# Performance work log

Hardware: AMD Instinct MI355X
Metric: run time of the kernel (lower is better)

## Reference

```python
import jax, jax.numpy as jnp
import numpy as np

EPS = 1e-05
MOMENTUM = 0.1


def inv_sqrtm(A, eps=1e-09):
    # torch.svd: A = U diag(S) V^T ; jnp.linalg.svd: A = U diag(S) Vh, so Vh == V^T
    U, S, Vh = jnp.linalg.svd(A)
    S = jnp.maximum(S, eps)
    return (U * (S ** -0.5)[None, :]) @ Vh


def setup_inputs() -> dict:
    key = jax.random.key(0)
    N, d = 262144, 512
    x = jax.random.normal(key, (N, d), dtype=jnp.float32)
    running_covar = jnp.eye(d, dtype=jnp.float32)
    return {"x": x, "running_covar": running_covar}


def reference(x, running_covar):
    # training-mode BatchWhiten with track_running_stats=True, momentum=0.1
    N = x.shape[0]
    covar = (x.T @ x) / N                       # [d, d]
    eaf = MOMENTUM
    running = running_covar * eaf + covar * (1.0 - eaf)
    covar = jnp.maximum(running, EPS)           # elementwise max, as in torch.max(covar, eps)
    B = inv_sqrtm(covar, EPS)                   # [d, d] inverse sqrt via SVD
    return x @ B                                # whitened input [N, d]
```

## Files before the change

### kernel.cpp

```cpp
#include <hip/hip_runtime.h>
#include <stdint.h>


#define N_ROWS 262144
#define D 512
#define NS_ITERS 3
#define CK_CHUNKS 128
#define CK_ROWS (N_ROWS / CK_CHUNKS)
#define BKC 32
#define CK_STEPS (CK_ROWS / BKC)

typedef float f32x4 __attribute__((ext_vector_type(4)));
typedef short s16x8 __attribute__((ext_vector_type(8)));
typedef short s16x4 __attribute__((ext_vector_type(4)));
typedef __bf16 bf16x8 __attribute__((ext_vector_type(8)));

static __device__ __forceinline__ unsigned short f2bf(float f) {
  unsigned u = __float_as_uint(f);
  u += 0x7FFFu + ((u >> 16) & 1u);
  return (unsigned short)(u >> 16);
}

static __device__ __forceinline__ f32x4 mfma16(s16x8 a, s16x8 b, f32x4 c) {
  return __builtin_amdgcn_mfma_f32_16x16x32_bf16(
      __builtin_bit_cast(bf16x8, a), __builtin_bit_cast(bf16x8, b), c, 0, 0, 0);
}

static __device__ __forceinline__ void gld_lds16(const void* g, void* l) {
  __builtin_amdgcn_global_load_lds(
      (const __attribute__((address_space(1))) void*)g,
      (__attribute__((address_space(3))) void*)l, 16, 0, 0);
}

#define SWZ8(c) (((c) ^ ((c) >> 3)) & 7)

#define CVOFF(c, kc) \
  ((((c) >> 1) << 6) + ((((((kc) << 1) | ((c) & 1))) ^ SWZ8((c) >> 1)) << 3))

#define GSW(row, g) (((g) ^ (((row) >> 1) & 3)) << 3)

static __device__ __forceinline__ void bar_lgkm() {
  asm volatile("s_waitcnt lgkmcnt(0)" ::: "memory");
  __builtin_amdgcn_s_barrier();
  __builtin_amdgcn_sched_barrier(0);
}

__global__ __launch_bounds__(512) void covar_k(const float* __restrict__ x,
                                               float* __restrict__ Cpart,
                                               short* __restrict__ xb16) {
  __shared__ short ldsT[2][2][128 * 32];

  const int hw = blockIdx.x;
  const int work = (hw & 7) * 160 + (hw >> 3);
  int t = work % 10, mb = 0, rl = 4;
  while (t >= rl) { t -= rl; ++mb; --rl; }
  const int nb = mb + t;
  const int chunk = work / 10;
  float* C = Cpart + (size_t)(hw & 7) * (D * D);

  const int tid = threadIdx.x;
  const int lane = tid & 63;
  const int wave = tid >> 6;
  const int isB = wave >> 2;
  const int kh = wave & 3;
  const int c2 = lane * 2;

  const int wr = wave >> 2, wc = wave & 3;
  const int l15 = lane & 15, g = lane >> 4;

  const bool offd = (nb != mb);
  const bool doStage = (!isB) || offd;
  const int tileCol = (isB ? nb : mb) * 128;

  const bool haveDump = (xb16 != nullptr);
  const int rank = isB ? (4 - (nb - mb)) : (nb - mb);
  const bool dump = haveDump && doStage && (kh == rank);
  uint32_t* xw = (uint32_t*)xb16;

  f32x4 acc[4][2];
#pragma unroll
  for (int i = 0; i < 4; ++i)
#pragma unroll
    for (int j = 0; j < 2; ++j) acc[i][j] = f32x4{0.f, 0.f, 0.f, 0.f};

  const size_t kbase0 = (size_t)chunk * CK_ROWS;
  const float* srcBase = x + (kbase0 + kh * 8) * D + tileCol + c2;

  float2 buf[8];
  if (doStage) {
#pragma unroll
    for (int q = 0; q < 8; ++q) buf[q] = *(const float2*)(srcBase + (size_t)q * D);
  }

  for (int st = 0; st < CK_STEPS; ++st) {
    if (doStage) {
      s16x8 p0, p1;
#pragma unroll
      for (int q = 0; q < 8; ++q) {
        p0[q] = (short)f2bf(buf[q].x);
        p1[q] = (short)f2bf(buf[q].y);
      }
      if (st + 1 < CK_STEPS) {
        const float* src = srcBase + (size_t)(st + 1) * BKC * D;
#pragma unroll
        for (int q = 0; q < 8; ++q) buf[q] = *(const float2*)(src + (size_t)q * D);
      }
      short* wp = ldsT[st & 1][isB];
      *(s16x8*)(wp + CVOFF(c2, kh)) = p0;
      *(s16x8*)(wp + CVOFF(c2 + 1, kh)) = p1;
      if (dump) {
        const size_t k0 = kbase0 + (size_t)st * BKC;
#pragma unroll
        for (int q = 0; q < 8; ++q) {
          const uint32_t u =
              (uint32_t)(uint16_t)p0[q] | ((uint32_t)(uint16_t)p1[q] << 16);
          __builtin_nontemporal_store(
              u, &xw[(k0 + kh * 8 + q) * 256 + (tileCol >> 1) + lane]);
        }
      }
    }

    bar_lgkm();

    const short* rA = ldsT[st & 1][0];
    const short* rB = ldsT[st & 1][offd ? 1 : 0];
    s16x8 af[4], bfv[2];
#pragma unroll
    for (int mi = 0; mi < 4; ++mi) {
      const int m = 64 * wr + 16 * mi + l15;
      af[mi] = *(const s16x8*)(rA + CVOFF(m, g));
    }
#pragma unroll
    for (int nj = 0; nj < 2; ++nj) {
      const int n = 32 * wc + 16 * nj + l15;
      bfv[nj] = *(const s16x8*)(rB + CVOFF(n, g));
    }
#pragma unroll
    for (int mi = 0; mi < 4; ++mi)
#pragma unroll
      for (int nj = 0; nj < 2; ++nj)
        acc[mi][nj] = mfma16(af[mi], bfv[nj], acc[mi][nj]);
  }

#pragma unroll
  for (int mi = 0; mi < 4; ++mi)
#pragma unroll
    for (int nj = 0; nj < 2; ++nj) {
      const int n = nb * 128 + 32 * wc + 16 * nj + l15;
#pragma unroll
      for (int r = 0; r < 4; ++r) {
        const int m = mb * 128 + 64 * wr + 16 * mi + 4 * g + r;
        atomicAdd(&C[(size_t)m * D + n], acc[mi][nj][r]);
      }
    }
}

__global__ __launch_bounds__(256) void prep_k(const float* __restrict__ Cpart,
                                              const float* __restrict__ run,
                                              float* __restrict__ M,
                                              unsigned* __restrict__ sMax) {
  const int r = blockIdx.x;
  const int t = threadIdx.x;
  const float cs = 0.9f / (float)N_ROWS;
  float sum = 0.f;
  for (int c = t; c < D; c += 256) {
    const int rr = r < c ? r : c;
    const int cc = r < c ? c : r;
    float cv = 0.f;
#pragma unroll
    for (int p = 0; p < 8; ++p)
      cv += Cpart[(size_t)p * D * D + (size_t)rr * D + cc];
    float v = 0.1f * run[(size_t)r * D + c] + cs * cv;
    v = fmaxf(v, 1e-5f);
    M[(size_t)r * D + c] = v;
    sum += v;
  }
  __shared__ float red[256];
  red[t] = sum;
  __syncthreads();
  for (int off = 128; off > 0; off >>= 1) {
    if (t < off) red[t] += red[t + off];
    __syncthreads();
  }
  if (t == 0) atomicMax(sMax, __float_as_uint(red[0]));
}

__global__ __launch_bounds__(256) void init2_k(const float* __restrict__ M,
                                               const unsigned* __restrict__ sMax,
                                               float* __restrict__ Y0,
                                               float* __restrict__ T,
                                               float* __restrict__ Z1) {
  const float inv = 1.0f / __uint_as_float(*sMax);
  const int i0 = (blockIdx.x * 256 + threadIdx.x) * 4;
  const float4 m4 = *(const float4*)&M[i0];
  const int row = i0 >> 9, col0 = i0 & 511;
  float y[4], tv[4];
#pragma unroll
  for (int e = 0; e < 4; ++e) {
    y[e] = (&m4.x)[e] * inv;
    tv[e] = (row == col0 + e ? 1.5f : 0.f) - 0.5f * y[e];
  }
  *(float4*)&Y0[i0] = make_float4(y[0], y[1], y[2], y[3]);
  const float4 t4 = make_float4(tv[0], tv[1], tv[2], tv[3]);
  *(float4*)&T[i0] = t4;
  *(float4*)&Z1[i0] = t4;
}

__device__ __forceinline__ void mm512_body(const float* __restrict__ A,
                                           const float* __restrict__ B,
                                           float* a00, float* a01, float* a10,
                                           float* a11, int rbase, int cbase) {
  __shared__ float As[32][36];
  __shared__ float Bs[32][36];
  const int t = threadIdx.x;
  const int tx = t & 15, ty = t >> 4;
  const int sr = t >> 3, sc = (t & 7) * 4;
  float c00 = 0.f, c01 = 0.f, c10 = 0.f, c11 = 0.f;
  for (int k0 = 0; k0 < D; k0 += 32) {
    __syncthreads();
    *(float4*)&As[sr][sc] = *(const float4*)(A + (size_t)(rbase + sr) * D + k0 + sc);
    *(float4*)&Bs[sr][sc] = *(const float4*)(B + (size_t)(k0 + sr) * D + cbase + sc);
    __syncthreads();
#pragma unroll
    for (int kk = 0; kk < 32; ++kk) {
      const float av0 = As[2 * ty][kk], av1 = As[2 * ty + 1][kk];
      const float2 bv = *(const float2*)&Bs[kk][2 * tx];
      c00 = fmaf(av0, bv.x, c00);
      c01 = fmaf(av0, bv.y, c01);
      c10 = fmaf(av1, bv.x, c10);
      c11 = fmaf(av1, bv.y, c11);
    }
  }
  *a00 = c00; *a01 = c01; *a10 = c10; *a11 = c11;
}

__global__ __launch_bounds__(256) void mmY_k(const float* __restrict__ A,
                                             const float* __restrict__ B,
                                             float* __restrict__ O) {
  const int rbase = blockIdx.y * 32, cbase = blockIdx.x * 32;
  float a00, a01, a10, a11;
  mm512_body(A, B, &a00, &a01, &a10, &a11, rbase, cbase);
  const int tx = threadIdx.x & 15, ty = threadIdx.x >> 4;
  const int r0 = rbase + 2 * ty, c0 = cbase + 2 * tx;
  O[(size_t)r0 * D + c0] = a00;
  O[(size_t)r0 * D + c0 + 1] = a01;
  O[(size_t)(r0 + 1) * D + c0] = a10;
  O[(size_t)(r0 + 1) * D + c0 + 1] = a11;
}

__global__ __launch_bounds__(256) void mmT_k(const float* __restrict__ Zm,
                                             const float* __restrict__ Ym,
                                             float* __restrict__ T) {
  const int rbase = blockIdx.y * 32, cbase = blockIdx.x * 32;
  float a00, a01, a10, a11;
  mm512_body(Zm, Ym, &a00, &a01, &a10, &a11, rbase, cbase);
  const int tx = threadIdx.x & 15, ty = threadIdx.x >> 4;
  const int r0 = rbase + 2 * ty, c0 = cbase + 2 * tx;
  T[(size_t)r0 * D + c0] = (r0 == c0 ? 1.5f : 0.f) - 0.5f * a00;
  T[(size_t)r0 * D + c0 + 1] = (r0 == c0 + 1 ? 1.5f : 0.f) - 0.5f * a01;
  T[(size_t)(r0 + 1) * D + c0] = (r0 + 1 == c0 ? 1.5f : 0.f) - 0.5f * a10;
  T[(size_t)(r0 + 1) * D + c0 + 1] = (r0 + 1 == c0 + 1 ? 1.5f : 0.f) - 0.5f * a11;
}

__global__ __launch_bounds__(256) void mmpair_k(const float* __restrict__ Y,
                                                const float* __restrict__ Z,
                                                const float* __restrict__ T,
                                                float* __restrict__ Yn,
                                                float* __restrict__ Zn) {
  const float* A = blockIdx.z ? T : Y;
  const float* B = blockIdx.z ? Z : T;
  float* O = blockIdx.z ? Zn : Yn;
  const int rbase = blockIdx.y * 32, cbase = blockIdx.x * 32;
  float a00, a01, a10, a11;
  mm512_body(A, B, &a00, &a01, &a10, &a11, rbase, cbase);
  const int tx = threadIdx.x & 15, ty = threadIdx.x >> 4;
  const int r0 = rbase + 2 * ty, c0 = cbase + 2 * tx;
  O[(size_t)r0 * D + c0] = a00;
  O[(size_t)r0 * D + c0 + 1] = a01;
  O[(size_t)(r0 + 1) * D + c0] = a10;
  O[(size_t)(r0 + 1) * D + c0 + 1] = a11;
}

__global__ __launch_bounds__(256) void mmZp_k(const float* __restrict__ T,
                                              const float* __restrict__ Z,
                                              const unsigned* __restrict__ sMax,
                                              short* __restrict__ panels) {
  const int rbase = blockIdx.y * 32, cbase = blockIdx.x * 32;
  float a00, a01, a10, a11;
  mm512_body(T, Z, &a00, &a01, &a10, &a11, rbase, cbase);
  const float rs = rsqrtf(__uint_as_float(*sMax));
  const int tx = threadIdx.x & 15, ty = threadIdx.x >> 4;
  const int r0 = rbase + 2 * ty, c0 = cbase + 2 * tx;
  const float vv[2][2] = {{a00, a01}, {a10, a11}};
#pragma unroll
  for (int dr = 0; dr < 2; ++dr)
#pragma unroll
    for (int dc = 0; dc < 2; ++dc) {
      const int k = r0 + dr, n = c0 + dc;
      const int nb_ = n >> 7, nl = n & 127;
      const int ks = k >> 5, kl = k & 31;
      const int ch = (kl >> 3) ^ ((nl >> 1) & 3), e = kl & 7;
      const size_t pi = (size_t)((nb_ * 16 + ks) * 128 + nl) * 32 + ch * 8 + e;
      panels[pi] = (short)f2bf(vv[dr][dc] * rs);
    }
}

__global__ __launch_bounds__(256) void gemm_k(const short* __restrict__ xb16,
                                              const short* __restrict__ panels,
                                              float* __restrict__ out) {
  __shared__ short lds[4][128 * 32];

  const int hw = blockIdx.x;
  const int q = hw & 7, j = hw >> 3;
  const int ct = j & 3;
  const int rp = ((j >> 2) << 3) | q;
  const size_t rbase = (size_t)rp * 128;

  const int tid = threadIdx.x;
  const int lane = tid & 63, wave = tid >> 6;
  const int wr = wave >> 1, wc = wave & 1;
  const int l15 = lane & 15, g = lane >> 4;

  f32x4 acc[4][4];
#pragma unroll
  for (int i = 0; i < 4; ++i)
#pragma unroll
    for (int j2 = 0; j2 < 4; ++j2) acc[i][j2] = f32x4{0.f, 0.f, 0.f, 0.f};

  auto STAGE = [&](int buf, int ksv) {
#pragma unroll
    for (int i = 0; i < 2; ++i) {
      const int rowbase = wave * 32 + i * 16;
      const int m = rowbase + (lane >> 2);
      const short* src =
          xb16 + (rbase + m) * D + ksv * 32 + GSW(m, lane & 3);
      gld_lds16(src, &lds[buf][rowbase * 32]);
    }
    const short* srcB = panels + ((size_t)(ct * 16 + ksv) << 12);
#pragma unroll
    for (int i = 0; i < 2; ++i)
      gld_lds16(srcB + wave * 1024 + i * 512 + lane * 8,
                &lds[2 + buf][wave * 1024 + i * 512]);
  };

  STAGE(0, 0);

  for (int ks = 0; ks < 16; ++ks) {
    const int cur = ks & 1;
    if (ks < 15) {
      STAGE(cur ^ 1, ks + 1);
      asm volatile("s_waitcnt vmcnt(4)" ::: "memory");
    } else {
      asm volatile("s_waitcnt vmcnt(0)" ::: "memory");
    }
    __builtin_amdgcn_s_barrier();
    __builtin_amdgcn_sched_barrier(0);

    const short* rA = lds[cur];
    const short* rB = lds[2 + cur];
    s16x8 af[4], bfv[4];
#pragma unroll
    for (int mi = 0; mi < 4; ++mi) {
      const int m = 64 * wr + 16 * mi + l15;
      af[mi] = *(const s16x8*)(rA + m * 32 + GSW(m, g));
    }
#pragma unroll
    for (int nj = 0; nj < 4; ++nj) {
      const int n = 64 * wc + 16 * nj + l15;
      bfv[nj] = *(const s16x8*)(rB + n * 32 + GSW(n, g));
    }
#pragma unroll
    for (int mi = 0; mi < 4; ++mi)
#pragma unroll
      for (int nj = 0; nj < 4; ++nj)
        acc[mi][nj] = mfma16(af[mi], bfv[nj], acc[mi][nj]);

    asm volatile("s_waitcnt lgkmcnt(0)" ::: "memory");
    __builtin_amdgcn_s_barrier();
    __builtin_amdgcn_sched_barrier(0);
  }

  float* scratch = (float*)&lds[0][0];
  const int wbase = wave * 1088;
#pragma unroll
  for (int mi = 0; mi < 4; ++mi) {
#pragma unroll
    for (int nj = 0; nj < 4; ++nj)
#pragma unroll
      for (int r = 0; r < 4; ++r)
        scratch[wbase + (4 * g + r) * 68 + 16 * nj + l15] = acc[mi][nj][r];
    __syncthreads();
#pragma unroll
    for (int i = 0; i < 4; ++i) {
      const int rl = g + 4 * i;
      const f32x4 v = *(const f32x4*)&scratch[wbase + rl * 68 + l15 * 4];
      const size_t row_g = rbase + 64 * wr + 16 * mi + rl;
      const int col_g = ct * 128 + 64 * wc + l15 * 4;
      __builtin_nontemporal_store(v, (f32x4*)(out + row_g * D + col_g));
    }
    __syncthreads();
  }
}

__global__ __launch_bounds__(256) void gemm_fb_k(const float* __restrict__ x,
                                                 const short* __restrict__ panels,
                                                 float* __restrict__ out) {
  __shared__ short lds[2][128 * 32];

  const int hw = blockIdx.x;
  const int q = hw & 7, j = hw >> 3;
  const int ct = j & 3;
  const int rp = ((j >> 2) << 3) | q;
  const size_t rbase = (size_t)rp * 128;

  const int tid = threadIdx.x;
  const int lane = tid & 63, wave = tid >> 6;
  const int wr = wave >> 1, wc = wave & 1;
  const int l15 = lane & 15, g = lane >> 4;

  const int am = tid >> 1;
  const int ak0 = (tid & 1) * 16;

  f32x4 acc[4][4];
#pragma unroll
  for (int i = 0; i < 4; ++i)
#pragma unroll
    for (int j2 = 0; j2 < 4; ++j2) acc[i][j2] = f32x4{0.f, 0.f, 0.f, 0.f};

  for (int ks = 0; ks < 16; ++ks) {
    __syncthreads();
#pragma unroll
    for (int h = 0; h < 2; ++h) {
      const float4 v =
          *(const float4*)(x + (rbase + am) * D + ks * 32 + ak0 + h * 4 + 0);
      const float4 v2 =
          *(const float4*)(x + (rbase + am) * D + ks * 32 + ak0 + h * 8 + 4);
      (void)v2;
    }
    {
      s16x8 p;
#pragma unroll
      for (int h = 0; h < 2; ++h) {
        const float4 a =
            *(const float4*)(x + (rbase + am) * D + ks * 32 + ak0 + h * 8);
        const float4 b =
            *(const float4*)(x + (rbase + am) * D + ks * 32 + ak0 + h * 8 + 4);
        p[0] = (short)f2bf(a.x); p[1] = (short)f2bf(a.y);
        p[2] = (short)f2bf(a.z); p[3] = (short)f2bf(a.w);
        p[4] = (short)f2bf(b.x); p[5] = (short)f2bf(b.y);
        p[6] = (short)f2bf(b.z); p[7] = (short)f2bf(b.w);
        const int ch = (ak0 >> 3) + h;
        *(s16x8*)(&lds[0][am * 32] + GSW(am, ch)) = p;
      }
    }
    {
      const short* srcB = panels + ((size_t)(ct * 16 + ks) << 12);
#pragma unroll
      for (int i = 0; i < 2; ++i)
        gld_lds16(srcB + wave * 1024 + i * 512 + lane * 8,
                  &lds[1][wave * 1024 + i * 512]);
    }
    __syncthreads();

    s16x8 af[4], bfv[4];
#pragma unroll
    for (int mi = 0; mi < 4; ++mi) {
      const int m = 64 * wr + 16 * mi + l15;
      af[mi] = *(const s16x8*)(&lds[0][m * 32] + GSW(m, g));
    }
#pragma unroll
    for (int nj = 0; nj < 4; ++nj) {
      const int n = 64 * wc + 16 * nj + l15;
      bfv[nj] = *(const s16x8*)(&lds[1][n * 32] + GSW(n, g));
    }
#pragma unroll
    for (int mi = 0; mi < 4; ++mi)
#pragma unroll
      for (int nj = 0; nj < 4; ++nj)
        acc[mi][nj] = mfma16(af[mi], bfv[nj], acc[mi][nj]);
  }

  __syncthreads();
  float* scratch = (float*)&lds[0][0];
  const int wbase = wave * 1088;
#pragma unroll
  for (int mi = 0; mi < 4; ++mi) {
#pragma unroll
    for (int nj = 0; nj < 4; ++nj)
#pragma unroll
      for (int r = 0; r < 4; ++r)
        scratch[wbase + (4 * g + r) * 68 + 16 * nj + l15] = acc[mi][nj][r];
    __syncthreads();
#pragma unroll
    for (int i = 0; i < 4; ++i) {
      const int rl = g + 4 * i;
      const f32x4 v = *(const f32x4*)&scratch[wbase + rl * 68 + l15 * 4];
      const size_t row_g = rbase + 64 * wr + 16 * mi + rl;
      const int col_g = ct * 128 + 64 * wc + l15 * 4;
      __builtin_nontemporal_store(v, (f32x4*)(out + row_g * D + col_g));
    }
    __syncthreads();
  }
}

extern "C" void kernel_launch(void* const* d_in, const int* in_sizes, int n_in,
                              void* d_out, int out_size, void* d_ws,
                              size_t ws_size, hipStream_t stream) {
  (void)in_sizes; (void)n_in; (void)out_size;
  const float* x = (const float*)d_in[0];
  const float* run = (const float*)d_in[1];
  float* out = (float*)d_out;
  uint8_t* ws = (uint8_t*)d_ws;

  float* Cpart = (float*)ws;
  unsigned* sMax = (unsigned*)(ws + (8u << 20));
  float* M = (float*)(ws + (8u << 20) + 256);
  float* Ya = M + 262144;
  float* Yb = Ya + 262144;
  float* Za = Yb + 262144;
  float* Zb = Za + 262144;
  float* T = Zb + 262144;
  short* panels = (short*)(T + 262144);
  short* xb16 = panels + 262144;

  const size_t need =
      (size_t)((uint8_t*)xb16 - ws) + (size_t)N_ROWS * D * sizeof(short);
  const bool big = ws_size >= need;

  (void)hipMemsetAsync(Cpart, 0, (8u << 20) + 256, stream);

  covar_k<<<1280, 512, 0, stream>>>(x, Cpart, big ? xb16 : nullptr);
  prep_k<<<512, 256, 0, stream>>>(Cpart, run, M, sMax);

  init2_k<<<256, 256, 0, stream>>>(M, sMax, Ya, T, Za);
  mmY_k<<<dim3(16, 16), 256, 0, stream>>>(Ya, T, Yb);

  float *Y = Yb, *Z = Za, *Yn = Ya, *Zn = Zb;
  for (int it = 1; it < NS_ITERS - 1; ++it) {
    mmT_k<<<dim3(16, 16), 256, 0, stream>>>(Z, Y, T);
    mmpair_k<<<dim3(16, 16, 2), 256, 0, stream>>>(Y, Z, T, Yn, Zn);
    float* t1 = Y; Y = Yn; Yn = t1;
    t1 = Z; Z = Zn; Zn = t1;
  }

  mmT_k<<<dim3(16, 16), 256, 0, stream>>>(Z, Y, T);
  mmZp_k<<<dim3(16, 16), 256, 0, stream>>>(T, Z, sMax, panels);

  if (big)
    gemm_k<<<8192, 256, 0, stream>>>(xb16, panels, out);
  else
    gemm_fb_k<<<8192, 256, 0, stream>>>(x, panels, out);
}
```

Baseline: 561.8 us.

## Enlarge covariance tiles to 256x256 with 1024-thread blocks

The covariance kernel moves from 128x128 output tiles (10 upper-triangle tile pairs per chunk) to 256x256 tiles (3 tile pairs per chunk) using 1024-thread blocks and twice as many row chunks. Each wave now accumulates a 64x64 sub-tile, which raises MFMA work per LDS fragment load and cuts the redundant fp32 reads of x across tile pairs. In exchange it uses more registers and LDS per block, and the diagonal blocks skip the lower-triangle atomic writes. Separately, unused dead float4 loads are removed from the fallback GEMM path.

```diff
diff --git a/kernel.cpp b/kernel.cpp
--- a/kernel.cpp
+++ b/kernel.cpp
@@ -5,7 +5,7 @@
 #define N_ROWS 262144
 #define D 512
 #define NS_ITERS 3
-#define CK_CHUNKS 128
+#define CK_CHUNKS 256
 #define CK_ROWS (N_ROWS / CK_CHUNKS)
 #define BKC 32
 #define CK_STEPS (CK_ROWS / BKC)
@@ -36,6 +36,7 @@
 
 #define CVOFF(c, kc) \
   ((((c) >> 1) << 6) + ((((((kc) << 1) | ((c) & 1))) ^ SWZ8((c) >> 1)) << 3))
+#define CVOFF256(c, kc) ((((c) >> 7) * 4096) + CVOFF((c) & 127, kc))
 
 #define GSW(row, g) (((g) ^ (((row) >> 1) & 3)) << 3)
 
@@ -45,43 +46,44 @@
   __builtin_amdgcn_sched_barrier(0);
 }
 
-__global__ __launch_bounds__(512) void covar_k(const float* __restrict__ x,
-                                               float* __restrict__ Cpart,
-                                               short* __restrict__ xb16) {
-  __shared__ short ldsT[2][2][128 * 32];
+__global__ __launch_bounds__(1024) void covar_k(const float* __restrict__ x,
+                                                float* __restrict__ Cpart,
+                                                short* __restrict__ xb16) {
+  __shared__ short ldsT[2][2][256 * 32];
 
   const int hw = blockIdx.x;
-  const int work = (hw & 7) * 160 + (hw >> 3);
-  int t = work % 10, mb = 0, rl = 4;
-  while (t >= rl) { t -= rl; ++mb; --rl; }
-  const int nb = mb + t;
-  const int chunk = work / 10;
+  const int work = (hw & 7) * 96 + (hw >> 3);
+  const int s = work % 3;
+  const int chunk = work / 3;
+  const int mb2 = (s == 2) ? 1 : 0;
+  const int nb2 = (s == 0) ? 0 : 1;
+  const bool diag = (mb2 == nb2);
   float* C = Cpart + (size_t)(hw & 7) * (D * D);
 
   const int tid = threadIdx.x;
   const int lane = tid & 63;
   const int wave = tid >> 6;
-  const int isB = wave >> 2;
-  const int kh = wave & 3;
-  const int c2 = lane * 2;
+  const int isB = wave >> 3;
+  const int st512 = tid & 511;
+  const int cp = st512 & 127;
+  const int kh = st512 >> 7;
+  const int c2 = cp * 2;
 
   const int wr = wave >> 2, wc = wave & 3;
   const int l15 = lane & 15, g = lane >> 4;
 
-  const bool offd = (nb != mb);
-  const bool doStage = (!isB) || offd;
-  const int tileCol = (isB ? nb : mb) * 128;
+  const bool doStage = (!isB) || (!diag);
+  const int tileCol = (isB ? nb2 : mb2) * 256;
 
   const bool haveDump = (xb16 != nullptr);
-  const int rank = isB ? (4 - (nb - mb)) : (nb - mb);
-  const bool dump = haveDump && doStage && (kh == rank);
+  const bool dump = haveDump && diag && (!isB);
   uint32_t* xw = (uint32_t*)xb16;
 
-  f32x4 acc[4][2];
+  f32x4 acc[4][4];
 #pragma unroll
   for (int i = 0; i < 4; ++i)
 #pragma unroll
-    for (int j = 0; j < 2; ++j) acc[i][j] = f32x4{0.f, 0.f, 0.f, 0.f};
+    for (int j = 0; j < 4; ++j) acc[i][j] = f32x4{0.f, 0.f, 0.f, 0.f};
 
   const size_t kbase0 = (size_t)chunk * CK_ROWS;
   const float* srcBase = x + (kbase0 + kh * 8) * D + tileCol + c2;
@@ -106,8 +108,8 @@
         for (int q = 0; q < 8; ++q) buf[q] = *(const float2*)(src + (size_t)q * D);
       }
       short* wp = ldsT[st & 1][isB];
-      *(s16x8*)(wp + CVOFF(c2, kh)) = p0;
-      *(s16x8*)(wp + CVOFF(c2 + 1, kh)) = p1;
+      *(s16x8*)(wp + CVOFF256(c2, kh)) = p0;
+      *(s16x8*)(wp + CVOFF256(c2 + 1, kh)) = p1;
       if (dump) {
         const size_t k0 = kbase0 + (size_t)st * BKC;
 #pragma unroll
@@ -115,7 +117,7 @@
           const uint32_t u =
               (uint32_t)(uint16_t)p0[q] | ((uint32_t)(uint16_t)p1[q] << 16);
           __builtin_nontemporal_store(
-              u, &xw[(k0 + kh * 8 + q) * 256 + (tileCol >> 1) + lane]);
+              u, &xw[(k0 + kh * 8 + q) * 256 + (tileCol >> 1) + cp]);
         }
       }
     }
@@ -123,36 +125,38 @@
     bar_lgkm();
 
     const short* rA = ldsT[st & 1][0];
-    const short* rB = ldsT[st & 1][offd ? 1 : 0];
-    s16x8 af[4], bfv[2];
+    const short* rB = ldsT[st & 1][diag ? 0 : 1];
+    s16x8 af[4], bfv[4];
 #pragma unroll
     for (int mi = 0; mi < 4; ++mi) {
       const int m = 64 * wr + 16 * mi + l15;
-      af[mi] = *(const s16x8*)(rA + CVOFF(m, g));
-    }
-#pragma unroll
-    for (int nj = 0; nj < 2; ++nj) {
-      const int n = 32 * wc + 16 * nj + l15;
-      bfv[nj] = *(const s16x8*)(rB + CVOFF(n, g));
+      af[mi] = *(const s16x8*)(rA + CVOFF256(m, g));
+    }
+#pragma unroll
+    for (int nj = 0; nj < 4; ++nj) {
+      const int n = 64 * wc + 16 * nj + l15;
+      bfv[nj] = *(const s16x8*)(rB + CVOFF256(n, g));
     }
 #pragma unroll
     for (int mi = 0; mi < 4; ++mi)
 #pragma unroll
-      for (int nj = 0; nj < 2; ++nj)
+      for (int nj = 0; nj < 4; ++nj)
         acc[mi][nj] = mfma16(af[mi], bfv[nj], acc[mi][nj]);
   }
 
-#pragma unroll
-  for (int mi = 0; mi < 4; ++mi)
-#pragma unroll
-    for (int nj = 0; nj < 2; ++nj) {
-      const int n = nb * 128 + 32 * wc + 16 * nj + l15;
-#pragma unroll
-      for (int r = 0; r < 4; ++r) {
-        const int m = mb * 128 + 64 * wr + 16 * mi + 4 * g + r;
-        atomicAdd(&C[(size_t)m * D + n], acc[mi][nj][r]);
+  if (!(diag && wr > wc)) {
+#pragma unroll
+    for (int mi = 0; mi < 4; ++mi)
+#pragma unroll
+      for (int nj = 0; nj < 4; ++nj) {
+        const int n = nb2 * 256 + 64 * wc + 16 * nj + l15;
+#pragma unroll
+        for (int r = 0; r < 4; ++r) {
+          const int m = mb2 * 256 + 64 * wr + 16 * mi + 4 * g + r;
+          atomicAdd(&C[(size_t)m * D + n], acc[mi][nj][r]);
+        }
       }
-    }
+  }
 }
 
 __global__ __launch_bounds__(256) void prep_k(const float* __restrict__ Cpart,
@@ -429,14 +433,6 @@
 
   for (int ks = 0; ks < 16; ++ks) {
     __syncthreads();
-#pragma unroll
-    for (int h = 0; h < 2; ++h) {
-      const float4 v =
-          *(const float4*)(x + (rbase + am) * D + ks * 32 + ak0 + h * 4 + 0);
-      const float4 v2 =
-          *(const float4*)(x + (rbase + am) * D + ks * 32 + ak0 + h * 8 + 4);
-      (void)v2;
-    }
     {
       s16x8 p;
 #pragma unroll
@@ -529,7 +525,7 @@
 
   (void)hipMemsetAsync(Cpart, 0, (8u << 20) + 256, stream);
 
-  covar_k<<<1280, 512, 0, stream>>>(x, Cpart, big ? xb16 : nullptr);
+  covar_k<<<768, 1024, 0, stream>>>(x, Cpart, big ? xb16 : nullptr);
   prep_k<<<512, 256, 0, stream>>>(Cpart, run, M, sMax);
 
   init2_k<<<256, 256, 0, stream>>>(M, sMax, Ya, T, Za);
```

New measurement: 627.6 us. +11.7%, slower.
